# Performance work log

Hardware: AMD Instinct MI355X
Metric: run time of the kernel (lower is better)

## Reference

```python
import jax, jax.numpy as jnp
import numpy as np

NUM_HEADS = 8
GROUPS = 32  # min(32, 512 // 4)
EPS = 1e-5


def group_norm(y, gamma, beta):
    B, C, L = y.shape
    yg = y.reshape(B, GROUPS, -1)  # [B, G, (C//G)*L]
    mu = yg.mean(-1, keepdims=True)
    var = yg.var(-1, keepdims=True)
    yn = ((yg - mu) * jax.lax.rsqrt(var + EPS)).reshape(B, C, L)
    return yn * gamma[:, None] + beta[:, None]


def setup_inputs() -> dict:
    key = jax.random.key(0)
    ks = jax.random.split(key, 5)
    B, C, L = 4, 512, 2048
    return {
        "x": jax.random.normal(ks[0], (B, C, L), dtype=jnp.float32),
        "Wqkv": jax.random.normal(ks[1], (3 * C, C), dtype=jnp.float32) * (C ** -0.5),
        "bqkv": jax.random.normal(ks[2], (3 * C,), dtype=jnp.float32) * 0.01,
        "Wproj": jax.random.normal(ks[3], (C, C), dtype=jnp.float32) * (C ** -0.5),
        "bproj": jax.random.normal(ks[4], (C,), dtype=jnp.float32) * 0.01,
        "gamma": jnp.ones((C,), dtype=jnp.float32),
        "beta": jnp.zeros((C,), dtype=jnp.float32),
    }


def reference(x, Wqkv, bqkv, Wproj, bproj, gamma, beta):
    B, C, L = x.shape
    H = NUM_HEADS
    D = C // H
    # 1x1 Conv1d == channel-mixing matmul
    qkv = jnp.einsum('oc,bcl->bol', Wqkv, x) + bqkv[:, None]  # [B, 3C, L]
    qkv = qkv.reshape(B, 3, H, D, L)
    q, k, v = qkv[:, 0], qkv[:, 1], qkv[:, 2]
    q = jnp.clip(q, -10.0, 10.0)
    k = jnp.clip(k, -10.0, 10.0)
    v = jnp.clip(v, -10.0, 10.0)
    scale = D ** -0.5
    attn = jnp.einsum('bhdi,bhdj->bhij', q, k) * scale  # [B, H, L, L]
    attn = jnp.clip(attn, -10.0, 10.0)
    attn = jax.nn.softmax(attn, axis=-1)
    # NaN fallback: replace whole attn with identity if any NaN (matches torch branch)
    has_nan = jnp.isnan(attn).any()
    attn = jnp.where(has_nan, jnp.eye(L, dtype=x.dtype), attn)
    out = jnp.einsum('bhij,bhdj->bhdi', attn, v)  # [B, H, D, L]
    out = out.reshape(B, C, L)
    out = jnp.einsum('oc,bcl->bol', Wproj, out) + bproj[:, None]
    return group_norm(out + x, gamma, beta)
```

## Files before the change

### kernel.cpp

```cpp
#include <hip/hip_runtime.h>
#include <cstddef>

#define B_ 4
#define C_ 512
#define L_ 2048

typedef __attribute__((ext_vector_type(8))) short  short8;
typedef __attribute__((ext_vector_type(4))) float  f32x4;
typedef __attribute__((ext_vector_type(4))) unsigned short us4;

#define AS1 __attribute__((address_space(1)))
#define AS3 __attribute__((address_space(3)))

__device__ __forceinline__ float clip10(float v){ return fminf(fmaxf(v,-10.0f),10.0f); }

__device__ __forceinline__ unsigned short f2bf(float f){
  union { float f; unsigned u; } v; v.f = f;
  unsigned r = v.u + 0x7fffu + ((v.u >> 16) & 1u);
  return (unsigned short)(r >> 16);
}
__device__ __forceinline__ unsigned pk_tr(float lo, float hi){
  return __builtin_amdgcn_perm(__float_as_uint(hi), __float_as_uint(lo), 0x07060302u);
}
__device__ __forceinline__ float bf2f(unsigned short u){
  return __uint_as_float(((unsigned)u)<<16);
}
__device__ __forceinline__ void gl16(const void* g, void* l){
  __builtin_amdgcn_global_load_lds((const AS1 unsigned*)g, (AS3 unsigned*)l, 16, 0, 0);
}
__device__ __forceinline__ void drain_dma(){
  asm volatile("s_waitcnt vmcnt(0)" ::: "memory");
}
__device__ __forceinline__ short8 mk8(unsigned a, unsigned b, unsigned c, unsigned d){
  union { unsigned u[4]; short8 s; } v;
  v.u[0]=a; v.u[1]=b; v.u[2]=c; v.u[3]=d;
  return v.s;
}

__global__ __launch_bounds__(256) void prep_k(
    const float* __restrict__ x, const float* __restrict__ Wq,
    const float* __restrict__ Wp, unsigned short* __restrict__ xT,
    unsigned short* __restrict__ Wqb, unsigned short* __restrict__ Wpb,
    float* __restrict__ part)
{
  const int blk = blockIdx.x;
  const int t = threadIdx.x;
  if (blk < 4096){
    __shared__ float tile[32][33];
    const int b = blk>>10, rem = blk&1023;
    const int c0 = (rem>>6)*32, l0 = (rem&63)*32;
    const int cr = t>>3, lc = (t&7)*4;
    const float4 v = *(const float4*)(x + ((size_t)b*C_ + c0+cr)*L_ + l0 + lc);
    tile[cr][lc]=v.x; tile[cr][lc+1]=v.y; tile[cr][lc+2]=v.z; tile[cr][lc+3]=v.w;
    __syncthreads();
    const int lr = t>>3, cc = (t&7)*4;
    const us4 o = { f2bf(tile[cc][lr]), f2bf(tile[cc+1][lr]),
                    f2bf(tile[cc+2][lr]), f2bf(tile[cc+3][lr]) };
    *(us4*)(xT + ((size_t)b*L_ + l0+lr)*C_ + c0 + cc) = o;
  } else if (blk < 5120){
    const int i = (blk-4096)*256 + t;
    const int NQ = 1536*512/4;
    const float* src; unsigned short* dst; int j;
    if (i < NQ){ src = Wq; dst = Wqb; j = i; }
    else       { src = Wp; dst = Wpb; j = i - NQ; }
    const float4 v = *(const float4*)(src + (size_t)j*4);
    const us4 o = { f2bf(v.x), f2bf(v.y), f2bf(v.z), f2bf(v.w) };
    *(us4*)(dst + (size_t)j*4) = o;
  } else {
    part[t] = 0.f;
  }
}

template<int MODE>
__global__ __launch_bounds__(256) void mfma_gemm(
    const unsigned short* __restrict__ Wb, const unsigned short* __restrict__ Bin,
    const float* __restrict__ bias, const float* __restrict__ xres,
    unsigned short* __restrict__ qT, unsigned short* __restrict__ kT,
    unsigned short* __restrict__ vN, float* __restrict__ yout,
    float* __restrict__ part)
{
  __shared__ unsigned short SA[128*64];
  __shared__ unsigned short SB[128*64];
  const int t = threadIdx.x;
  const int b = blockIdx.z;
  const int mb = blockIdx.y, n0 = blockIdx.x*128, m0 = mb*128;
  const int lane = t&63, w = t>>6, wm = w>>1, wn = w&1;
  const int n = lane&15, q4 = lane>>4;
  const bool VSWAP = (MODE==0) && (mb>=8);

  f32x4 acc[4][4];
#pragma unroll
  for (int i=0;i<4;i++)
#pragma unroll
    for (int j=0;j<4;j++) acc[i][j] = (f32x4){0.f,0.f,0.f,0.f};

  const unsigned short* Arow = Wb + (size_t)m0*512;
  const unsigned short* Brow = Bin + ((size_t)b*L_ + n0)*512;

  for (int kt=0; kt<8; kt++){
    const int k0 = kt*64;
    __syncthreads();
#pragma unroll
    for (int i=0;i<4;i++){
      const int ch = t + 256*i;
      const int row = ch>>3, lc = (ch&7) ^ (row&7);
      gl16(Arow + (size_t)row*512 + k0 + lc*8, &SA[ch*8]);
      gl16(Brow + (size_t)row*512 + k0 + lc*8, &SB[ch*8]);
    }
    drain_dma();
    __syncthreads();
#pragma unroll
    for (int kk=0;kk<2;kk++){
      short8 aF[4], bF[4];
      const int pc = ((kk*4+q4) ^ (n&7))*8;
#pragma unroll
      for (int mt=0;mt<4;mt++) aF[mt] = *(const short8*)&SA[(wm*64+mt*16+n)*64 + pc];
#pragma unroll
      for (int nt=0;nt<4;nt++) bF[nt] = *(const short8*)&SB[(wn*64+nt*16+n)*64 + pc];
      if (VSWAP){
#pragma unroll
        for (int mt=0;mt<4;mt++)
#pragma unroll
          for (int nt=0;nt<4;nt++)
            acc[mt][nt] = __builtin_amdgcn_mfma_f32_16x16x32_bf16(bF[nt], aF[mt], acc[mt][nt], 0,0,0);
      } else {
#pragma unroll
        for (int mt=0;mt<4;mt++)
#pragma unroll
          for (int nt=0;nt<4;nt++)
            acc[mt][nt] = __builtin_amdgcn_mfma_f32_16x16x32_bf16(aF[mt], bF[nt], acc[mt][nt], 0,0,0);
      }
    }
  }

  const float QS = 0.180336880f;
  if (VSWAP){
#pragma unroll
    for (int mt=0;mt<4;mt++){
      const int o = m0 + wm*64 + mt*16 + n;
      const float bv = bias[o];
#pragma unroll
      for (int nt=0;nt<4;nt++){
        const int p = ((nt>>1)<<2) | ((q4&1)<<3) | ((q4>>1)<<4) | ((nt&1)<<5);
        const int l = n0 + wn*64 + p;
        const float r0=clip10(acc[mt][nt][0]+bv), r1=clip10(acc[mt][nt][1]+bv),
                    r2=clip10(acc[mt][nt][2]+bv), r3=clip10(acc[mt][nt][3]+bv);
        const us4 ov = { f2bf(r0), f2bf(r1), f2bf(r2), f2bf(r3) };
        *(us4*)&vN[((size_t)b*512 + (o-1024))*L_ + l] = ov;
      }
    }
    return;
  }
#pragma unroll
  for (int mt=0;mt<4;mt++){
    const int obase = m0 + wm*64 + mt*16 + q4*4;
    const float b0=bias[obase], b1=bias[obase+1], b2=bias[obase+2], b3=bias[obase+3];
    float gs=0.f, gq=0.f;
#pragma unroll
    for (int nt=0;nt<4;nt++){
      const int l = n0 + wn*64 + nt*16 + n;
      float r0=acc[mt][nt][0]+b0, r1=acc[mt][nt][1]+b1,
            r2=acc[mt][nt][2]+b2, r3=acc[mt][nt][3]+b3;
      if (MODE==0){
        r0=clip10(r0); r1=clip10(r1); r2=clip10(r2); r3=clip10(r3);
        const int typ = mb>>2;
        const int oin = obase - typ*512;
        if (typ==0){ r0*=QS; r1*=QS; r2*=QS; r3*=QS; }
        unsigned short* dst = (typ==0) ? qT : kT;
        const us4 o = { f2bf(r0), f2bf(r1), f2bf(r2), f2bf(r3) };
        *(us4*)&dst[((size_t)b*L_ + l)*512 + oin] = o;
      } else {
        const float* xp = xres + ((size_t)b*512 + obase)*L_ + l;
        const float y0=r0+xp[0], y1=r1+xp[(size_t)L_],
                    y2=r2+xp[(size_t)2*L_], y3=r3+xp[(size_t)3*L_];
        float* dst = yout + ((size_t)b*512 + obase)*L_ + l;
        dst[0]=y0; dst[(size_t)L_]=y1; dst[(size_t)2*L_]=y2; dst[(size_t)3*L_]=y3;
        gs += (y0+y1)+(y2+y3);
        gq += (y0*y0+y1*y1)+(y2*y2+y3*y3);
      }
    }
    if (MODE==1){
#pragma unroll
      for (int off=1; off<64; off<<=1){
        gs += __shfl_xor(gs, off);
        gq += __shfl_xor(gq, off);
      }
      if (lane==0){
        const int g = mb*8 + wm*4 + mt;
        atomicAdd(&part[(b*32+g)*2+0], gs);
        atomicAdd(&part[(b*32+g)*2+1], gq);
      }
    }
  }
}

#define OPX 68

__global__ __launch_bounds__(512,4) void attn_v13(
    const unsigned short* __restrict__ qT, const unsigned short* __restrict__ kT,
    const unsigned short* __restrict__ vN,
    unsigned short* __restrict__ attnT)
{
  __shared__ unsigned short smem[16384];
  const int t  = threadIdx.x;
  const int id  = blockIdx.x;
  const int xcd = id & 7, s = id >> 3;
  const int pr  = xcd*4 + (s & 3);
  const int i0  = (s >> 2) * 128;
  const int h   = pr & 7, b = pr >> 3;
  const int lane = t&63, w = t>>6, n = lane&15, q4 = lane>>4;

  const unsigned short* kb0 = kT + (size_t)b*L_*512 + h*64;
  const unsigned short* vb  = vN + ((size_t)b*512 + h*64)*L_;

  short8 qf[2];
#pragma unroll
  for (int kk=0; kk<2; kk++)
    qf[kk] = *(const short8*)(qT + ((size_t)b*L_ + i0 + w*16 + n)*512
                                 + h*64 + kk*32 + q4*8);

  short8 ones;
#pragma unroll
  for (int i=0;i<8;i++) ones[i] = (short)0x3F80;

  f32x4 oacc[4];
  f32x4 oden = (f32x4){0.f,0.f,0.f,0.f};
#pragma unroll
  for (int dt=0;dt<4;dt++) oacc[dt]=(f32x4){0.f,0.f,0.f,0.f};

  const float LIM = 14.4269504089f;

  {
    const int ch = t, row = ch>>3, lc = (ch&7)^(row&7);
    gl16(kb0 + (size_t)row*512 + lc*8, &smem[ch*8]);
    gl16(vb  + (size_t)row*L_ + lc*8,  &smem[4096 + ch*8]);
  }
  drain_dma();
  __syncthreads();

  for (int j0=0; j0<L_; j0+=64){
    const int cur = (j0>>6)&1;
    const unsigned short* sk = &smem[cur*8192];
    const unsigned short* sv = &smem[cur*8192 + 4096];

    if (j0+64 < L_){
      const int nb = cur^1;
      const int ch = t, row = ch>>3, lc = (ch&7)^(row&7);
      gl16(kb0 + (size_t)(j0+64+row)*512 + lc*8, &smem[nb*8192 + ch*8]);
      gl16(vb  + (size_t)row*L_ + j0+64 + lc*8,  &smem[nb*8192+4096 + ch*8]);
    }

    f32x4 sacc[4];
#pragma unroll
    for (int jt=0;jt<4;jt++) sacc[jt]=(f32x4){0.f,0.f,0.f,0.f};
#pragma unroll
    for (int kk=0;kk<2;kk++){
      const int pc = ((kk*4+q4) ^ (n&7))*8;
      short8 aK[4];
#pragma unroll
      for (int jt=0;jt<4;jt++) aK[jt] = *(const short8*)&sk[(jt*16+n)*64 + pc];
#pragma unroll
      for (int jt=0;jt<4;jt++)
        sacc[jt] = __builtin_amdgcn_mfma_f32_16x16x32_bf16(aK[jt], qf[kk], sacc[jt], 0,0,0);
    }

    unsigned pw[4][2];
#pragma unroll
    for (int jt=0;jt<4;jt++){
      const float e0 = __builtin_amdgcn_exp2f(__builtin_amdgcn_fmed3f(sacc[jt][0],-LIM,LIM));
      const float e1 = __builtin_amdgcn_exp2f(__builtin_amdgcn_fmed3f(sacc[jt][1],-LIM,LIM));
      const float e2 = __builtin_amdgcn_exp2f(__builtin_amdgcn_fmed3f(sacc[jt][2],-LIM,LIM));
      const float e3 = __builtin_amdgcn_exp2f(__builtin_amdgcn_fmed3f(sacc[jt][3],-LIM,LIM));
      pw[jt][0] = pk_tr(e0,e1);
      pw[jt][1] = pk_tr(e2,e3);
    }

#pragma unroll
    for (int kk=0;kk<2;kk++){
      const int pcv = ((kk*4+q4) ^ (n&7))*8;
      short8 bV[4];
#pragma unroll
      for (int dt=0;dt<4;dt++) bV[dt] = *(const short8*)&sv[(dt*16+n)*64 + pcv];
      const short8 pA = mk8(pw[kk][0], pw[kk][1], pw[kk+2][0], pw[kk+2][1]);
#pragma unroll
      for (int dt=0;dt<4;dt++)
        oacc[dt] = __builtin_amdgcn_mfma_f32_16x16x32_bf16(pA, bV[dt], oacc[dt], 0,0,0);
      oden = __builtin_amdgcn_mfma_f32_16x16x32_bf16(pA, ones, oden, 0,0,0);
    }
    drain_dma();
    __syncthreads();
  }

  float inv[4];
#pragma unroll
  for (int r=0;r<4;r++) inv[r] = 1.0f/oden[r];

  unsigned short* sb = smem;
#pragma unroll
  for (int dt=0;dt<4;dt++)
#pragma unroll
    for (int r=0;r<4;r++)
      sb[(w*16 + q4*4 + r)*OPX + dt*16 + n] = f2bf(oacc[dt][r]*inv[r]);
#pragma unroll
  for (int it=0; it<4; it++){
    const int chunk = it*64 + lane;
    const int row = chunk>>4, c4 = (chunk&15)*4;
    const us4 ov = *(const us4*)&sb[(w*16 + row)*OPX + c4];
    *(us4*)&attnT[((size_t)b*L_ + i0 + w*16 + row)*512 + h*64 + c4] = ov;
  }
}

__global__ __launch_bounds__(256) void gn_apply(
    const float* __restrict__ y, const float* __restrict__ part,
    const float* __restrict__ gamma, const float* __restrict__ beta,
    float* __restrict__ out)
{
  const int blk = blockIdx.x;
  const int b = blk>>7, g = (blk>>2)&31, s = blk&3;
  const float sum = part[(b*32+g)*2+0];
  const float sq  = part[(b*32+g)*2+1];
  const float mu = sum*(1.0f/32768.0f);
  const float rs = rsqrtf(sq*(1.0f/32768.0f) - mu*mu + 1e-5f);
  const size_t base = ((size_t)b*C_ + g*16)*L_ + s*512;
  const int t = threadIdx.x;
#pragma unroll
  for (int i=0;i<8;i++){
    const int e = i*256 + t;
    const int row = e>>7;
    const size_t off = base + (size_t)row*L_ + (e&127)*4;
    const int c = g*16 + row;
    const float ga = gamma[c], be = beta[c];
    const float4 vy=*(const float4*)(y+off);
    float4 r;
    r.x=(vy.x-mu)*rs*ga+be;
    r.y=(vy.y-mu)*rs*ga+be;
    r.z=(vy.z-mu)*rs*ga+be;
    r.w=(vy.w-mu)*rs*ga+be;
    *(float4*)(out+off)=r;
  }
}

extern "C" void kernel_launch(void* const* d_in, const int* in_sizes, int n_in,
                              void* d_out, int out_size, void* d_ws, size_t ws_size,
                              hipStream_t stream)
{
  (void)in_sizes; (void)n_in; (void)out_size; (void)ws_size;
  const float* x     = (const float*)d_in[0];
  const float* Wqkv  = (const float*)d_in[1];
  const float* bqkv  = (const float*)d_in[2];
  const float* Wproj = (const float*)d_in[3];
  const float* bproj = (const float*)d_in[4];
  const float* gamma = (const float*)d_in[5];
  const float* beta  = (const float*)d_in[6];
  float* out = (float*)d_out;
  char* ws = (char*)d_ws;

  const size_t MB = 1024*1024;
  unsigned short* qT    = (unsigned short*)(ws);
  unsigned short* kT    = (unsigned short*)(ws +  8*MB);
  unsigned short* vN    = (unsigned short*)(ws + 16*MB);
  unsigned short* attnT = (unsigned short*)(ws + 24*MB);
  unsigned short* xT    = (unsigned short*)(ws + 32*MB);
  unsigned short* Wqb   = (unsigned short*)(ws + 42*MB);
  unsigned short* Wpb   = (unsigned short*)(ws + 44*MB);
  float*          y     = (float*)        (ws + 45*MB);
  float*          part  = (float*)        (ws + 61*MB);

  prep_k      <<<dim3(5121),   256,0,stream>>>(x, Wqkv, Wproj, xT, Wqb, Wpb, part);
  mfma_gemm<0><<<dim3(16,12,4),256,0,stream>>>(Wqb, xT,    bqkv , nullptr, qT,kT,vN, nullptr, nullptr);
  attn_v13    <<<dim3(512),    512,0,stream>>>(qT, kT, vN, attnT);
  mfma_gemm<1><<<dim3(16, 4,4),256,0,stream>>>(Wpb, attnT, bproj, x, nullptr,nullptr,nullptr, y, part);
  gn_apply    <<<dim3(512),    256,0,stream>>>(y, part, gamma, beta, out);
}
```

Before: 178.1 us.

## Fuse projection GEMM and group-norm apply via cooperative grid sync

Splits the templated GEMM into a QKV kernel and a projection kernel. The projection kernel now keeps the residual-added outputs in registers, accumulates group statistics with atomics, does a cooperative grid-wide sync, and then applies group norm directly to the output. This drops the fp32 intermediate y buffer, its write and re-read, and one kernel launch. In exchange it pays for a grid barrier over 256 blocks and needs a cooperative launch, which requires every block to be resident at the same time.

```diff
diff --git a/kernel.cpp b/kernel.cpp
--- a/kernel.cpp
+++ b/kernel.cpp
@@ -1,5 +1,8 @@
 #include <hip/hip_runtime.h>
+#include <hip/hip_cooperative_groups.h>
 #include <cstddef>
+
+namespace cg = cooperative_groups;
 
 #define B_ 4
 #define C_ 512
@@ -71,13 +74,11 @@
   }
 }
 
-template<int MODE>
-__global__ __launch_bounds__(256) void mfma_gemm(
+__global__ __launch_bounds__(256) void qkv_gemm(
     const unsigned short* __restrict__ Wb, const unsigned short* __restrict__ Bin,
-    const float* __restrict__ bias, const float* __restrict__ xres,
+    const float* __restrict__ bias,
     unsigned short* __restrict__ qT, unsigned short* __restrict__ kT,
-    unsigned short* __restrict__ vN, float* __restrict__ yout,
-    float* __restrict__ part)
+    unsigned short* __restrict__ vN)
 {
   __shared__ unsigned short SA[128*64];
   __shared__ unsigned short SB[128*64];
@@ -86,7 +87,7 @@
   const int mb = blockIdx.y, n0 = blockIdx.x*128, m0 = mb*128;
   const int lane = t&63, w = t>>6, wm = w>>1, wn = w&1;
   const int n = lane&15, q4 = lane>>4;
-  const bool VSWAP = (MODE==0) && (mb>=8);
+  const bool VSWAP = (mb>=8);
 
   f32x4 acc[4][4];
 #pragma unroll
@@ -155,41 +156,124 @@
   for (int mt=0;mt<4;mt++){
     const int obase = m0 + wm*64 + mt*16 + q4*4;
     const float b0=bias[obase], b1=bias[obase+1], b2=bias[obase+2], b3=bias[obase+3];
-    float gs=0.f, gq=0.f;
 #pragma unroll
     for (int nt=0;nt<4;nt++){
       const int l = n0 + wn*64 + nt*16 + n;
-      float r0=acc[mt][nt][0]+b0, r1=acc[mt][nt][1]+b1,
-            r2=acc[mt][nt][2]+b2, r3=acc[mt][nt][3]+b3;
-      if (MODE==0){
-        r0=clip10(r0); r1=clip10(r1); r2=clip10(r2); r3=clip10(r3);
-        const int typ = mb>>2;
-        const int oin = obase - typ*512;
-        if (typ==0){ r0*=QS; r1*=QS; r2*=QS; r3*=QS; }
-        unsigned short* dst = (typ==0) ? qT : kT;
-        const us4 o = { f2bf(r0), f2bf(r1), f2bf(r2), f2bf(r3) };
-        *(us4*)&dst[((size_t)b*L_ + l)*512 + oin] = o;
-      } else {
-        const float* xp = xres + ((size_t)b*512 + obase)*L_ + l;
-        const float y0=r0+xp[0], y1=r1+xp[(size_t)L_],
-                    y2=r2+xp[(size_t)2*L_], y3=r3+xp[(size_t)3*L_];
-        float* dst = yout + ((size_t)b*512 + obase)*L_ + l;
-        dst[0]=y0; dst[(size_t)L_]=y1; dst[(size_t)2*L_]=y2; dst[(size_t)3*L_]=y3;
-        gs += (y0+y1)+(y2+y3);
-        gq += (y0*y0+y1*y1)+(y2*y2+y3*y3);
-      }
-    }
-    if (MODE==1){
-#pragma unroll
-      for (int off=1; off<64; off<<=1){
-        gs += __shfl_xor(gs, off);
-        gq += __shfl_xor(gq, off);
-      }
-      if (lane==0){
-        const int g = mb*8 + wm*4 + mt;
-        atomicAdd(&part[(b*32+g)*2+0], gs);
-        atomicAdd(&part[(b*32+g)*2+1], gq);
-      }
+      float r0=clip10(acc[mt][nt][0]+b0), r1=clip10(acc[mt][nt][1]+b1),
+            r2=clip10(acc[mt][nt][2]+b2), r3=clip10(acc[mt][nt][3]+b3);
+      const int typ = mb>>2;
+      const int oin = obase - typ*512;
+      if (typ==0){ r0*=QS; r1*=QS; r2*=QS; r3*=QS; }
+      unsigned short* dst = (typ==0) ? qT : kT;
+      const us4 o = { f2bf(r0), f2bf(r1), f2bf(r2), f2bf(r3) };
+      *(us4*)&dst[((size_t)b*L_ + l)*512 + oin] = o;
+    }
+  }
+}
+
+__global__ __launch_bounds__(256) void proj_gn(
+    const unsigned short* __restrict__ Wb, const unsigned short* __restrict__ Bin,
+    const float* __restrict__ bias, const float* __restrict__ xres,
+    float* __restrict__ part, const float* __restrict__ gamma,
+    const float* __restrict__ beta, float* __restrict__ out)
+{
+  __shared__ unsigned short SA[128*64];
+  __shared__ unsigned short SB[128*64];
+  const int t = threadIdx.x;
+  const int b = blockIdx.z;
+  const int mb = blockIdx.y, n0 = blockIdx.x*128, m0 = mb*128;
+  const int lane = t&63, w = t>>6, wm = w>>1, wn = w&1;
+  const int n = lane&15, q4 = lane>>4;
+
+  f32x4 acc[4][4];
+#pragma unroll
+  for (int i=0;i<4;i++)
+#pragma unroll
+    for (int j=0;j<4;j++) acc[i][j] = (f32x4){0.f,0.f,0.f,0.f};
+
+  const unsigned short* Arow = Wb + (size_t)m0*512;
+  const unsigned short* Brow = Bin + ((size_t)b*L_ + n0)*512;
+
+  for (int kt=0; kt<8; kt++){
+    const int k0 = kt*64;
+    __syncthreads();
+#pragma unroll
+    for (int i=0;i<4;i++){
+      const int ch = t + 256*i;
+      const int row = ch>>3, lc = (ch&7) ^ (row&7);
+      gl16(Arow + (size_t)row*512 + k0 + lc*8, &SA[ch*8]);
+      gl16(Brow + (size_t)row*512 + k0 + lc*8, &SB[ch*8]);
+    }
+    drain_dma();
+    __syncthreads();
+#pragma unroll
+    for (int kk=0;kk<2;kk++){
+      short8 aF[4], bF[4];
+      const int pc = ((kk*4+q4) ^ (n&7))*8;
+#pragma unroll
+      for (int mt=0;mt<4;mt++) aF[mt] = *(const short8*)&SA[(wm*64+mt*16+n)*64 + pc];
+#pragma unroll
+      for (int nt=0;nt<4;nt++) bF[nt] = *(const short8*)&SB[(wn*64+nt*16+n)*64 + pc];
+#pragma unroll
+      for (int mt=0;mt<4;mt++)
+#pragma unroll
+        for (int nt=0;nt<4;nt++)
+          acc[mt][nt] = __builtin_amdgcn_mfma_f32_16x16x32_bf16(aF[mt], bF[nt], acc[mt][nt], 0,0,0);
+    }
+  }
+
+#pragma unroll
+  for (int mt=0;mt<4;mt++){
+    const int obase = m0 + wm*64 + mt*16 + q4*4;
+    const float b0=bias[obase], b1=bias[obase+1], b2=bias[obase+2], b3=bias[obase+3];
+    float gs=0.f, gq=0.f;
+#pragma unroll
+    for (int nt=0;nt<4;nt++){
+      const int l = n0 + wn*64 + nt*16 + n;
+      const float* xp = xres + ((size_t)b*512 + obase)*L_ + l;
+      const float y0=acc[mt][nt][0]+b0+xp[0],
+                  y1=acc[mt][nt][1]+b1+xp[(size_t)L_],
+                  y2=acc[mt][nt][2]+b2+xp[(size_t)2*L_],
+                  y3=acc[mt][nt][3]+b3+xp[(size_t)3*L_];
+      acc[mt][nt][0]=y0; acc[mt][nt][1]=y1; acc[mt][nt][2]=y2; acc[mt][nt][3]=y3;
+      gs += (y0+y1)+(y2+y3);
+      gq += (y0*y0+y1*y1)+(y2*y2+y3*y3);
+    }
+#pragma unroll
+    for (int off=1; off<64; off<<=1){
+      gs += __shfl_xor(gs, off);
+      gq += __shfl_xor(gq, off);
+    }
+    if (lane==0){
+      const int g = mb*8 + wm*4 + mt;
+      atomicAdd(&part[(b*32+g)*2+0], gs);
+      atomicAdd(&part[(b*32+g)*2+1], gq);
+    }
+  }
+
+  __threadfence();
+  cg::this_grid().sync();
+
+#pragma unroll
+  for (int mt=0;mt<4;mt++){
+    const int g = mb*8 + wm*4 + mt;
+    const float sum = part[(b*32+g)*2+0];
+    const float sq  = part[(b*32+g)*2+1];
+    const float mu = sum*(1.0f/32768.0f);
+    const float rs = rsqrtf(sq*(1.0f/32768.0f) - mu*mu + 1e-5f);
+    const int obase = m0 + wm*64 + mt*16 + q4*4;
+    const float ga0=gamma[obase]*rs,   ga1=gamma[obase+1]*rs,
+                ga2=gamma[obase+2]*rs, ga3=gamma[obase+3]*rs;
+    const float be0=beta[obase]   - mu*ga0, be1=beta[obase+1] - mu*ga1,
+                be2=beta[obase+2] - mu*ga2, be3=beta[obase+3] - mu*ga3;
+#pragma unroll
+    for (int nt=0;nt<4;nt++){
+      const int l = n0 + wn*64 + nt*16 + n;
+      float* dst = out + ((size_t)b*512 + obase)*L_ + l;
+      dst[0]            = acc[mt][nt][0]*ga0 + be0;
+      dst[(size_t)L_]   = acc[mt][nt][1]*ga1 + be1;
+      dst[(size_t)2*L_] = acc[mt][nt][2]*ga2 + be2;
+      dst[(size_t)3*L_] = acc[mt][nt][3]*ga3 + be3;
     }
   }
 }
@@ -307,36 +391,6 @@
     const int row = chunk>>4, c4 = (chunk&15)*4;
     const us4 ov = *(const us4*)&sb[(w*16 + row)*OPX + c4];
     *(us4*)&attnT[((size_t)b*L_ + i0 + w*16 + row)*512 + h*64 + c4] = ov;
-  }
-}
-
-__global__ __launch_bounds__(256) void gn_apply(
-    const float* __restrict__ y, const float* __restrict__ part,
-    const float* __restrict__ gamma, const float* __restrict__ beta,
-    float* __restrict__ out)
-{
-  const int blk = blockIdx.x;
-  const int b = blk>>7, g = (blk>>2)&31, s = blk&3;
-  const float sum = part[(b*32+g)*2+0];
-  const float sq  = part[(b*32+g)*2+1];
-  const float mu = sum*(1.0f/32768.0f);
-  const float rs = rsqrtf(sq*(1.0f/32768.0f) - mu*mu + 1e-5f);
-  const size_t base = ((size_t)b*C_ + g*16)*L_ + s*512;
-  const int t = threadIdx.x;
-#pragma unroll
-  for (int i=0;i<8;i++){
-    const int e = i*256 + t;
-    const int row = e>>7;
-    const size_t off = base + (size_t)row*L_ + (e&127)*4;
-    const int c = g*16 + row;
-    const float ga = gamma[c], be = beta[c];
-    const float4 vy=*(const float4*)(y+off);
-    float4 r;
-    r.x=(vy.x-mu)*rs*ga+be;
-    r.y=(vy.y-mu)*rs*ga+be;
-    r.z=(vy.z-mu)*rs*ga+be;
-    r.w=(vy.w-mu)*rs*ga+be;
-    *(float4*)(out+off)=r;
   }
 }
 
@@ -363,12 +417,18 @@
   unsigned short* xT    = (unsigned short*)(ws + 32*MB);
   unsigned short* Wqb   = (unsigned short*)(ws + 42*MB);
   unsigned short* Wpb   = (unsigned short*)(ws + 44*MB);
-  float*          y     = (float*)        (ws + 45*MB);
   float*          part  = (float*)        (ws + 61*MB);
 
-  prep_k      <<<dim3(5121),   256,0,stream>>>(x, Wqkv, Wproj, xT, Wqb, Wpb, part);
-  mfma_gemm<0><<<dim3(16,12,4),256,0,stream>>>(Wqb, xT,    bqkv , nullptr, qT,kT,vN, nullptr, nullptr);
-  attn_v13    <<<dim3(512),    512,0,stream>>>(qT, kT, vN, attnT);
-  mfma_gemm<1><<<dim3(16, 4,4),256,0,stream>>>(Wpb, attnT, bproj, x, nullptr,nullptr,nullptr, y, part);
-  gn_apply    <<<dim3(512),    256,0,stream>>>(y, part, gamma, beta, out);
-}
+  prep_k  <<<dim3(5121),   256,0,stream>>>(x, Wqkv, Wproj, xT, Wqb, Wpb, part);
+  qkv_gemm<<<dim3(16,12,4),256,0,stream>>>(Wqb, xT, bqkv, qT, kT, vN);
+  attn_v13<<<dim3(512),    512,0,stream>>>(qT, kT, vN, attnT);
+
+  {
+    const unsigned short* Wpb_c = Wpb;
+    const unsigned short* attnT_c = attnT;
+    void* args[] = { (void*)&Wpb_c, (void*)&attnT_c, (void*)&bproj, (void*)&x,
+                     (void*)&part, (void*)&gamma, (void*)&beta, (void*)&out };
+    hipLaunchCooperativeKernel((const void*)proj_gn, dim3(16,4,4), dim3(256),
+                               args, 0, stream);
+  }
+}
```

After: 249.8 us. 1.4x slower.
